# Performance work log

Measured on AMD Instinct MI355X. Metric: run time of the kernel, lower is better.

Reference implementation:

```python
import jax, jax.numpy as jnp
import numpy as np

T = 100000
HDIM = 16
UDIM = 7
HID = 64
DT = 5.0 / 60.0  # 5 minutes in hours


def setup_inputs() -> dict:
    key = jax.random.key(0)
    ks = jax.random.split(key, 12)

    def lin(k, out_d, in_d):
        # torch nn.Linear default init: U(-1/sqrt(in), 1/sqrt(in)); scale-equivalent gaussian is fine for a numeric reference
        bound = 1.0 / np.sqrt(in_d)
        return jax.random.uniform(k, (out_d, in_d), jnp.float32, -bound, bound)

    return {
        "U": jax.random.normal(ks[0], (T, UDIM), jnp.float32),
        "W1": lin(ks[1], HID, HDIM + UDIM),
        "b1": jnp.zeros((HID,), jnp.float32),
        "W2": lin(ks[2], HID, HID),
        "b2": jnp.zeros((HID,), jnp.float32),
        "W3": lin(ks[3], HDIM, HID),
        "b3": jnp.zeros((HDIM,), jnp.float32),
        "wd": lin(ks[4], 1, HDIM).reshape(HDIM),
        "bd": jnp.zeros((), jnp.float32),
        "wt": lin(ks[5], 1, HDIM).reshape(HDIM),
        "bt": jnp.zeros((), jnp.float32),
        "wc": lin(ks[6], 1, HDIM).reshape(HDIM),
        "bc": jnp.zeros((), jnp.float32),
        "h0": jnp.zeros((HDIM,), jnp.float32),
    }


def reference(U, W1, b1, W2, b2, W3, b3, wd, bd, wt, bt, wc, bc, h0):
    dt = jnp.float32(DT)

    def step(h, u):
        # readout at current state (before the Euler step), matching the torch loop order
        d = h @ wd + bd
        tx = h @ wt + bt
        ll = h @ wc + bc
        x = jnp.concatenate([h, u])                    # (HDIM+UDIM,)
        z = jnp.tanh(W1 @ x + b1)                      # (HID,)
        z = jnp.tanh(W2 @ z + b2)                      # (HID,)
        dh = W3 @ z + b3                               # (HDIM,)
        return h + dh * dt, (d, tx, ll)

    hT, (delay, taxi, loglam) = jax.lax.scan(step, h0, U)
    return delay, taxi, loglam, hT.reshape(1, HDIM)
```

## Files before the change

### kernel.cpp

```cpp
#include <hip/hip_runtime.h>

typedef float v2f __attribute__((ext_vector_type(2)));

#define T_STEPS 100000
#define UDIM 7
#define NCHUNK 1562
#define TAIL 32
#define ZSTR 68

__device__ __forceinline__ float tanh_fast(float x) {
    float e = __expf(2.0f * x);
    return 1.0f - 2.0f * __builtin_amdgcn_rcpf(e + 1.0f);
}

__device__ __forceinline__ float readlane_f(float v, int l) {
    return __int_as_float(__builtin_amdgcn_readlane(__float_as_int(v), l));
}

template <int CTRL>
__device__ __forceinline__ float dpp_f(float v) {
    return __int_as_float(__builtin_amdgcn_update_dpp(
        0, __float_as_int(v), CTRL, 0xF, 0xF, true));
}

__global__ __launch_bounds__(64) __attribute__((amdgpu_waves_per_eu(1, 1)))
void node_scan(const float* __restrict__ U,
               const float* __restrict__ W1, const float* __restrict__ b1,
               const float* __restrict__ W2, const float* __restrict__ b2,
               const float* __restrict__ W3, const float* __restrict__ b3,
               const float* __restrict__ wd, const float* __restrict__ bd,
               const float* __restrict__ wt, const float* __restrict__ bt,
               const float* __restrict__ wc, const float* __restrict__ bc,
               const float* __restrict__ h0,
               float* __restrict__ out)
{
    const int lane = threadIdx.x;
    const int g = lane >> 2;
    const int q = lane & 3;
    const float dt = (float)(5.0 / 60.0);

    __shared__ __align__(16) float zbuf[64];
    __shared__ __align__(16) float ubuf[2 * 64 * 8];
    __shared__ __align__(16) float zhist[64 * ZSTR];
    __shared__ __align__(16) float cbuf[3 * 64];
    __shared__ __align__(16) float Msh[64 * 64];

    float w1h[16];
#pragma unroll
    for (int j = 0; j < 16; ++j) w1h[j] = W1[lane * 23 + j];
    v2f W1up[3];
#pragma unroll
    for (int j = 0; j < 3; ++j) {
        W1up[j].x = W1[lane * 23 + 16 + 2 * j];
        W1up[j].y = W1[lane * 23 + 17 + 2 * j];
    }
    const float W1u6 = W1[lane * 23 + 22];
    const float b1r = b1[lane];
    const float b2r = b2[lane];

    v2f W2p[4][8];
#pragma unroll
    for (int d = 0; d < 4; ++d) {
        const int orow = (g << 2) | (q ^ d);
        const float* w2r = W2 + orow * 64 + q * 16;
#pragma unroll
        for (int j = 0; j < 8; ++j) W2p[d][j] = (v2f){ w2r[2 * j], w2r[2 * j + 1] };
    }

    for (int c = 0; c < 64; ++c) {
        float acc = 0.f;
#pragma unroll
        for (int k = 0; k < 16; ++k) acc = fmaf(w1h[k], W3[k * 64 + c], acc);
        Msh[lane * 64 + c] = acc;
    }
    __syncthreads();
    v2f Mp[4][8];
#pragma unroll
    for (int d = 0; d < 4; ++d) {
        const int orow = (g << 2) | (q ^ d);
        const float* mr = Msh + orow * 64 + q * 16;
#pragma unroll
        for (int j = 0; j < 8; ++j) Mp[d][j] = (v2f){ mr[2 * j], mr[2 * j + 1] };
    }
    float m3od = 0.f;
#pragma unroll
    for (int k = 0; k < 16; ++k) m3od = fmaf(w1h[k], b3[k], m3od);

    {
        float cd = 0.f, ct = 0.f, cc = 0.f;
        for (int k = 0; k < 16; ++k) {
            const float w3v = W3[k * 64 + lane];
            cd = fmaf(wd[k], w3v, cd);
            ct = fmaf(wt[k], w3v, ct);
            cc = fmaf(wc[k], w3v, cc);
        }
        cbuf[lane] = cd; cbuf[64 + lane] = ct; cbuf[128 + lane] = cc;
    }
    float rbD = 0.f, rbT = 0.f, rbC = 0.f;
    float rchD = bd[0], rchT = bt[0], rchC = bc[0];
    for (int k = 0; k < 16; ++k) {
        rbD = fmaf(wd[k], b3[k], rbD);  rchD = fmaf(wd[k], h0[k], rchD);
        rbT = fmaf(wt[k], b3[k], rbT);  rchT = fmaf(wt[k], h0[k], rchT);
        rbC = fmaf(wc[k], b3[k], rbC);  rchC = fmaf(wc[k], h0[k], rchC);
    }
    rbD *= dt; rbT *= dt; rbC *= dt;

    float A = 0.f;
    for (int k = 0; k < 16; ++k) A = fmaf(w1h[k], h0[k], A);
    float zacc = 0.f;

#pragma unroll
    for (int r = 0; r < UDIM; ++r) {
        int flat = r * 64 + lane;
        int s = flat / 7, c = flat % 7;
        ubuf[s * 8 + c] = U[flat];
    }
    ubuf[lane * 8 + 7] = 0.f;
    ubuf[512 + lane * 8 + 7] = 0.f;
    __syncthreads();

    float tmp[UDIM];
#pragma unroll
    for (int r = 0; r < UDIM; ++r) tmp[r] = U[448 + r * 64 + lane];

    float uacc;
    {
        float4 ua = *(const float4*)&ubuf[0];
        float4 ub = *(const float4*)&ubuf[4];
        v2f v0 = __builtin_elementwise_fma(W1up[0], (v2f){ua.x, ua.y}, (v2f){0.f, 0.f});
        v0 = __builtin_elementwise_fma(W1up[1], (v2f){ua.z, ua.w}, v0);
        v0 = __builtin_elementwise_fma(W1up[2], (v2f){ub.x, ub.y}, v0);
        uacc = v0.x + v0.y + fmaf(W1u6, ub.z, b1r);
    }

    auto step = [&](int li, int uoff) {
        const float z1 = tanh_fast(A + uacc);
        zbuf[lane] = z1;
        float4 s0 = *(const float4*)&zbuf[q * 16 + 0];
        float4 s1 = *(const float4*)&zbuf[q * 16 + 4];
        float4 s2 = *(const float4*)&zbuf[q * 16 + 8];
        float4 s3 = *(const float4*)&zbuf[q * 16 + 12];

        float4 una = *(const float4*)&ubuf[uoff];
        float4 unb = *(const float4*)&ubuf[uoff + 4];

        v2f e0 = {s0.x, s0.y}, e1 = {s0.z, s0.w};
        v2f e2 = {s1.x, s1.y}, e3 = {s1.z, s1.w};
        v2f e4 = {s2.x, s2.y}, e5 = {s2.z, s2.w};
        v2f e6 = {s3.x, s3.y}, e7 = {s3.z, s3.w};
        v2f c0 = {b2r, 0.f}, c1 = {0.f, 0.f}, c2 = {0.f, 0.f}, c3 = {0.f, 0.f};
        c0 = __builtin_elementwise_fma(W2p[0][0], e0, c0);
        c1 = __builtin_elementwise_fma(W2p[1][0], e0, c1);
        c2 = __builtin_elementwise_fma(W2p[2][0], e0, c2);
        c3 = __builtin_elementwise_fma(W2p[3][0], e0, c3);
        c0 = __builtin_elementwise_fma(W2p[0][1], e1, c0);
        c1 = __builtin_elementwise_fma(W2p[1][1], e1, c1);
        c2 = __builtin_elementwise_fma(W2p[2][1], e1, c2);
        c3 = __builtin_elementwise_fma(W2p[3][1], e1, c3);
        c0 = __builtin_elementwise_fma(W2p[0][2], e2, c0);
        c1 = __builtin_elementwise_fma(W2p[1][2], e2, c1);
        c2 = __builtin_elementwise_fma(W2p[2][2], e2, c2);
        c3 = __builtin_elementwise_fma(W2p[3][2], e2, c3);
        c0 = __builtin_elementwise_fma(W2p[0][3], e3, c0);
        c1 = __builtin_elementwise_fma(W2p[1][3], e3, c1);
        c2 = __builtin_elementwise_fma(W2p[2][3], e3, c2);
        c3 = __builtin_elementwise_fma(W2p[3][3], e3, c3);
        c0 = __builtin_elementwise_fma(W2p[0][4], e4, c0);
        c1 = __builtin_elementwise_fma(W2p[1][4], e4, c1);
        c2 = __builtin_elementwise_fma(W2p[2][4], e4, c2);
        c3 = __builtin_elementwise_fma(W2p[3][4], e4, c3);
        c0 = __builtin_elementwise_fma(W2p[0][5], e5, c0);
        c1 = __builtin_elementwise_fma(W2p[1][5], e5, c1);
        c2 = __builtin_elementwise_fma(W2p[2][5], e5, c2);
        c3 = __builtin_elementwise_fma(W2p[3][5], e5, c3);
        c0 = __builtin_elementwise_fma(W2p[0][6], e6, c0);
        c1 = __builtin_elementwise_fma(W2p[1][6], e6, c1);
        c2 = __builtin_elementwise_fma(W2p[2][6], e6, c2);
        c3 = __builtin_elementwise_fma(W2p[3][6], e6, c3);
        c0 = __builtin_elementwise_fma(W2p[0][7], e7, c0);
        c1 = __builtin_elementwise_fma(W2p[1][7], e7, c1);
        c2 = __builtin_elementwise_fma(W2p[2][7], e7, c2);
        c3 = __builtin_elementwise_fma(W2p[3][7], e7, c3);
        const float P0 = c0.x + c0.y;
        const float P1 = c1.x + c1.y;
        const float P2 = c2.x + c2.y;
        const float P3 = c3.x + c3.y;
        const float Q = P0 + dpp_f<0xB1>(P1) + dpp_f<0x4E>(P2) + dpp_f<0x1B>(P3);
        const float z2 = tanh_fast(Q);
        zhist[li * ZSTR + lane] = z2;
        const float* zrow = &zhist[li * ZSTR + q * 16];
        float4 t0 = *(const float4*)&zrow[0];
        float4 t1 = *(const float4*)&zrow[4];
        float4 t2 = *(const float4*)&zrow[8];
        float4 t3 = *(const float4*)&zrow[12];
        zacc += z2;

        v2f f0 = {t0.x, t0.y}, f1 = {t0.z, t0.w};
        v2f f2 = {t1.x, t1.y}, f3 = {t1.z, t1.w};
        v2f f4 = {t2.x, t2.y}, f5 = {t2.z, t2.w};
        v2f f6 = {t3.x, t3.y}, f7 = {t3.z, t3.w};
        v2f m0 = {m3od, 0.f}, m1 = {0.f, 0.f}, m2 = {0.f, 0.f}, m3 = {0.f, 0.f};
        m0 = __builtin_elementwise_fma(Mp[0][0], f0, m0);
        m1 = __builtin_elementwise_fma(Mp[1][0], f0, m1);
        m2 = __builtin_elementwise_fma(Mp[2][0], f0, m2);
        m3 = __builtin_elementwise_fma(Mp[3][0], f0, m3);
        m0 = __builtin_elementwise_fma(Mp[0][1], f1, m0);
        m1 = __builtin_elementwise_fma(Mp[1][1], f1, m1);
        m2 = __builtin_elementwise_fma(Mp[2][1], f1, m2);
        m3 = __builtin_elementwise_fma(Mp[3][1], f1, m3);
        m0 = __builtin_elementwise_fma(Mp[0][2], f2, m0);
        m1 = __builtin_elementwise_fma(Mp[1][2], f2, m1);
        m2 = __builtin_elementwise_fma(Mp[2][2], f2, m2);
        m3 = __builtin_elementwise_fma(Mp[3][2], f2, m3);
        m0 = __builtin_elementwise_fma(Mp[0][3], f3, m0);
        m1 = __builtin_elementwise_fma(Mp[1][3], f3, m1);
        m2 = __builtin_elementwise_fma(Mp[2][3], f3, m2);
        m3 = __builtin_elementwise_fma(Mp[3][3], f3, m3);
        m0 = __builtin_elementwise_fma(Mp[0][4], f4, m0);
        m1 = __builtin_elementwise_fma(Mp[1][4], f4, m1);
        m2 = __builtin_elementwise_fma(Mp[2][4], f4, m2);
        m3 = __builtin_elementwise_fma(Mp[3][4], f4, m3);
        m0 = __builtin_elementwise_fma(Mp[0][5], f5, m0);
        m1 = __builtin_elementwise_fma(Mp[1][5], f5, m1);
        m2 = __builtin_elementwise_fma(Mp[2][5], f5, m2);
        m3 = __builtin_elementwise_fma(Mp[3][5], f5, m3);
        m0 = __builtin_elementwise_fma(Mp[0][6], f6, m0);
        m1 = __builtin_elementwise_fma(Mp[1][6], f6, m1);
        m2 = __builtin_elementwise_fma(Mp[2][6], f6, m2);
        m3 = __builtin_elementwise_fma(Mp[3][6], f6, m3);
        m0 = __builtin_elementwise_fma(Mp[0][7], f7, m0);
        m1 = __builtin_elementwise_fma(Mp[1][7], f7, m1);
        m2 = __builtin_elementwise_fma(Mp[2][7], f7, m2);
        m3 = __builtin_elementwise_fma(Mp[3][7], f7, m3);
        const float R0 = m0.x + m0.y;
        const float R1 = m1.x + m1.y;
        const float R2 = m2.x + m2.y;
        const float R3 = m3.x + m3.y;
        const float R = R0 + dpp_f<0xB1>(R1) + dpp_f<0x4E>(R2) + dpp_f<0x1B>(R3);
        A = fmaf(dt, R, A);

        v2f uv = __builtin_elementwise_fma(W1up[0], (v2f){una.x, una.y}, (v2f){0.f, 0.f});
        uv = __builtin_elementwise_fma(W1up[1], (v2f){una.z, una.w}, uv);
        uv = __builtin_elementwise_fma(W1up[2], (v2f){unb.x, unb.y}, uv);
        uacc = uv.x + uv.y + fmaf(W1u6, unb.z, b1r);
    };

    auto batch = [&](int t0) {
        const float* zr = &zhist[lane * ZSTR];
        v2f sd = {0.f, 0.f}, st = {0.f, 0.f}, sc = {0.f, 0.f};
#pragma unroll
        for (int qq = 0; qq < 32; ++qq) {
            v2f zv = *(const v2f*)&zr[2 * qq];
            sd = __builtin_elementwise_fma(*(const v2f*)&cbuf[2 * qq],       zv, sd);
            st = __builtin_elementwise_fma(*(const v2f*)&cbuf[64 + 2 * qq],  zv, st);
            sc = __builtin_elementwise_fma(*(const v2f*)&cbuf[128 + 2 * qq], zv, sc);
        }
        float Sd = sd.x + sd.y, St = st.x + st.y, Sc = sc.x + sc.y;
        const float oD = Sd, oT = St, oC = Sc;
#pragma unroll
        for (int dl = 1; dl < 64; dl <<= 1) {
            float ud = __shfl_up(Sd, dl, 64);
            float ut = __shfl_up(St, dl, 64);
            float uc = __shfl_up(Sc, dl, 64);
            if (lane >= dl) { Sd += ud; St += ut; Sc += uc; }
        }
        const int t = t0 + lane;
        if (t < T_STEPS) {
            const float fl = (float)lane;
            out[t]               = fmaf(dt, Sd - oD, rchD) + fl * rbD;
            out[T_STEPS + t]     = fmaf(dt, St - oT, rchT) + fl * rbT;
            out[2 * T_STEPS + t] = fmaf(dt, Sc - oC, rchC) + fl * rbC;
        }
        rchD = fmaf(dt, readlane_f(Sd, 63), rchD) + 64.f * rbD;
        rchT = fmaf(dt, readlane_f(St, 63), rchT) + 64.f * rbT;
        rchC = fmaf(dt, readlane_f(Sc, 63), rchC) + 64.f * rbC;
    };

    for (int cb = 0; cb < NCHUNK; ++cb) {
        const int buf512  = 512 * (cb & 1);
        const int other   = 512 * ((cb + 1) & 1);
#pragma unroll
        for (int r = 0; r < UDIM; ++r) {
            int flat = r * 64 + lane;
            int s = flat / 7, c = flat % 7;
            ubuf[other + s * 8 + c] = tmp[r];
        }
        const int base = (cb + 2) * 448;
#pragma unroll
        for (int r = 0; r < UDIM; ++r) {
            int idx = base + r * 64 + lane;
            if (idx > T_STEPS * UDIM - 1) idx = T_STEPS * UDIM - 1;
            tmp[r] = U[idx];
        }
#pragma unroll 8
        for (int li = 0; li < 64; ++li) {
            const int uoff = (li < 63) ? buf512 + (li + 1) * 8 : other;
            step(li, uoff);
        }
        batch(cb * 64);
    }
    for (int li = 0; li < TAIL; ++li) step(li, (li + 1) * 8);
    batch(NCHUNK * 64);

    zbuf[lane] = zacc;
    float4 za[16];
#pragma unroll
    for (int qq = 0; qq < 16; ++qq) za[qq] = *(const float4*)&zbuf[qq * 4];
    const int row = lane & 15;
    const float* w3r = W3 + row * 64;
    float h0a = 0.f, h1a = 0.f;
#pragma unroll
    for (int qq = 0; qq < 16; ++qq) {
        h0a = fmaf(w3r[4 * qq + 0], za[qq].x, h0a);
        h1a = fmaf(w3r[4 * qq + 1], za[qq].y, h1a);
        h0a = fmaf(w3r[4 * qq + 2], za[qq].z, h0a);
        h1a = fmaf(w3r[4 * qq + 3], za[qq].w, h1a);
    }
    const float hT = h0[row] + dt * (h0a + h1a) + (float)T_STEPS * dt * b3[row];
    if (lane < 16) out[3 * T_STEPS + lane] = hT;
}

extern "C" void kernel_launch(void* const* d_in, const int* in_sizes, int n_in,
                              void* d_out, int out_size, void* d_ws, size_t ws_size,
                              hipStream_t stream) {
    const float* U  = (const float*)d_in[0];
    const float* W1 = (const float*)d_in[1];
    const float* b1 = (const float*)d_in[2];
    const float* W2 = (const float*)d_in[3];
    const float* b2 = (const float*)d_in[4];
    const float* W3 = (const float*)d_in[5];
    const float* b3 = (const float*)d_in[6];
    const float* wd = (const float*)d_in[7];
    const float* bd = (const float*)d_in[8];
    const float* wt = (const float*)d_in[9];
    const float* bt = (const float*)d_in[10];
    const float* wc = (const float*)d_in[11];
    const float* bc = (const float*)d_in[12];
    const float* h0 = (const float*)d_in[13];
    (void)in_sizes; (void)n_in; (void)out_size; (void)d_ws; (void)ws_size;

    node_scan<<<dim3(1), dim3(64), 0, stream>>>(U, W1, b1, W2, b2, W3, b3,
                                                wd, bd, wt, bt, wc, bc, h0,
                                                (float*)d_out);
}
```

Before: 28.55 ms.

## Split recurrence and readout/prefetch into producer-consumer warps with LDS flags

Launches two wavefronts: wave 0 runs only the serial recurrent steps, while wave 1 prefetches U into a triple-buffered LDS ring and computes the readout prefix-scan and output stores for the previous chunk from a double-buffered z history. Workgroup-scope atomic flags with s_sleep spin loops replace the in-line prefetch and batch work. This takes readout and global-memory latency off the critical serial path. The cost is spin-wait overhead, extra LDS, and a risk that the flag handshake stalls the recurrence wave.

```diff
diff --git a/kernel.cpp b/kernel.cpp
--- a/kernel.cpp
+++ b/kernel.cpp
@@ -7,6 +7,7 @@
 #define NCHUNK 1562
 #define TAIL 32
 #define ZSTR 68
+#define ZH (64 * ZSTR)
 
 __device__ __forceinline__ float tanh_fast(float x) {
     float e = __expf(2.0f * x);
@@ -23,7 +24,7 @@
         0, __float_as_int(v), CTRL, 0xF, 0xF, true));
 }
 
-__global__ __launch_bounds__(64) __attribute__((amdgpu_waves_per_eu(1, 1)))
+__global__ __launch_bounds__(128) __attribute__((amdgpu_waves_per_eu(1, 1)))
 void node_scan(const float* __restrict__ U,
                const float* __restrict__ W1, const float* __restrict__ b1,
                const float* __restrict__ W2, const float* __restrict__ b2,
@@ -34,59 +35,51 @@
                const float* __restrict__ h0,
                float* __restrict__ out)
 {
-    const int lane = threadIdx.x;
+    const int tid  = threadIdx.x;
+    const int wv   = tid >> 6;
+    const int lane = tid & 63;
     const int g = lane >> 2;
     const int q = lane & 3;
     const float dt = (float)(5.0 / 60.0);
 
     __shared__ __align__(16) float zbuf[64];
-    __shared__ __align__(16) float ubuf[2 * 64 * 8];
-    __shared__ __align__(16) float zhist[64 * ZSTR];
+    __shared__ __align__(16) float ubuf[3 * 512];
+    __shared__ __align__(16) float zhist[2 * ZH];
     __shared__ __align__(16) float cbuf[3 * 64];
     __shared__ __align__(16) float Msh[64 * 64];
-
-    float w1h[16];
-#pragma unroll
-    for (int j = 0; j < 16; ++j) w1h[j] = W1[lane * 23 + j];
-    v2f W1up[3];
-#pragma unroll
-    for (int j = 0; j < 3; ++j) {
-        W1up[j].x = W1[lane * 23 + 16 + 2 * j];
-        W1up[j].y = W1[lane * 23 + 17 + 2 * j];
-    }
-    const float W1u6 = W1[lane * 23 + 22];
-    const float b1r = b1[lane];
-    const float b2r = b2[lane];
-
+    __shared__ int flg[4];
+
+    if (tid == 0) { flg[0] = 0; flg[1] = 3; flg[2] = 0; }
+
+    float w1h[16]; v2f W1up[3]; float W1u6 = 0.f, b1r = 0.f, b2r = 0.f;
     v2f W2p[4][8];
-#pragma unroll
-    for (int d = 0; d < 4; ++d) {
-        const int orow = (g << 2) | (q ^ d);
-        const float* w2r = W2 + orow * 64 + q * 16;
-#pragma unroll
-        for (int j = 0; j < 8; ++j) W2p[d][j] = (v2f){ w2r[2 * j], w2r[2 * j + 1] };
-    }
-
-    for (int c = 0; c < 64; ++c) {
-        float acc = 0.f;
-#pragma unroll
-        for (int k = 0; k < 16; ++k) acc = fmaf(w1h[k], W3[k * 64 + c], acc);
-        Msh[lane * 64 + c] = acc;
-    }
-    __syncthreads();
-    v2f Mp[4][8];
-#pragma unroll
-    for (int d = 0; d < 4; ++d) {
-        const int orow = (g << 2) | (q ^ d);
-        const float* mr = Msh + orow * 64 + q * 16;
-#pragma unroll
-        for (int j = 0; j < 8; ++j) Mp[d][j] = (v2f){ mr[2 * j], mr[2 * j + 1] };
-    }
-    float m3od = 0.f;
-#pragma unroll
-    for (int k = 0; k < 16; ++k) m3od = fmaf(w1h[k], b3[k], m3od);
-
-    {
+    float rbD = 0.f, rbT = 0.f, rbC = 0.f, rchD = 0.f, rchT = 0.f, rchC = 0.f;
+
+    if (wv == 0) {
+#pragma unroll
+        for (int j = 0; j < 16; ++j) w1h[j] = W1[lane * 23 + j];
+#pragma unroll
+        for (int j = 0; j < 3; ++j) {
+            W1up[j].x = W1[lane * 23 + 16 + 2 * j];
+            W1up[j].y = W1[lane * 23 + 17 + 2 * j];
+        }
+        W1u6 = W1[lane * 23 + 22];
+        b1r = b1[lane];
+        b2r = b2[lane];
+#pragma unroll
+        for (int d = 0; d < 4; ++d) {
+            const int orow = (g << 2) | (q ^ d);
+            const float* w2r = W2 + orow * 64 + q * 16;
+#pragma unroll
+            for (int j = 0; j < 8; ++j) W2p[d][j] = (v2f){ w2r[2 * j], w2r[2 * j + 1] };
+        }
+        for (int c = 0; c < 64; ++c) {
+            float acc = 0.f;
+#pragma unroll
+            for (int k = 0; k < 16; ++k) acc = fmaf(w1h[k], W3[k * 64 + c], acc);
+            Msh[lane * 64 + c] = acc;
+        }
+    } else {
         float cd = 0.f, ct = 0.f, cc = 0.f;
         for (int k = 0; k < 16; ++k) {
             const float w3v = W3[k * 64 + lane];
@@ -95,229 +88,256 @@
             cc = fmaf(wc[k], w3v, cc);
         }
         cbuf[lane] = cd; cbuf[64 + lane] = ct; cbuf[128 + lane] = cc;
+        rchD = bd[0]; rchT = bt[0]; rchC = bc[0];
+        for (int k = 0; k < 16; ++k) {
+            rbD = fmaf(wd[k], b3[k], rbD);  rchD = fmaf(wd[k], h0[k], rchD);
+            rbT = fmaf(wt[k], b3[k], rbT);  rchT = fmaf(wt[k], h0[k], rchT);
+            rbC = fmaf(wc[k], b3[k], rbC);  rchC = fmaf(wc[k], h0[k], rchC);
+        }
+        rbD *= dt; rbT *= dt; rbC *= dt;
+#pragma unroll
+        for (int c = 0; c < 3; ++c) {
+            const int base = c * 448, dst = c * 512;
+#pragma unroll
+            for (int r = 0; r < UDIM; ++r) {
+                int flat = r * 64 + lane;
+                int s = flat / 7, cc2 = flat % 7;
+                ubuf[dst + s * 8 + cc2] = U[base + flat];
+            }
+            ubuf[dst + lane * 8 + 7] = 0.f;
+        }
     }
-    float rbD = 0.f, rbT = 0.f, rbC = 0.f;
-    float rchD = bd[0], rchT = bt[0], rchC = bc[0];
-    for (int k = 0; k < 16; ++k) {
-        rbD = fmaf(wd[k], b3[k], rbD);  rchD = fmaf(wd[k], h0[k], rchD);
-        rbT = fmaf(wt[k], b3[k], rbT);  rchT = fmaf(wt[k], h0[k], rchT);
-        rbC = fmaf(wc[k], b3[k], rbC);  rchC = fmaf(wc[k], h0[k], rchC);
+    __syncthreads();
+
+    if (wv == 0) {
+        v2f Mp[4][8];
+#pragma unroll
+        for (int d = 0; d < 4; ++d) {
+            const int orow = (g << 2) | (q ^ d);
+            const float* mr = Msh + orow * 64 + q * 16;
+#pragma unroll
+            for (int j = 0; j < 8; ++j) Mp[d][j] = (v2f){ mr[2 * j], mr[2 * j + 1] };
+        }
+        float m3od = 0.f;
+#pragma unroll
+        for (int k = 0; k < 16; ++k) m3od = fmaf(w1h[k], b3[k], m3od);
+        float A = 0.f;
+        for (int k = 0; k < 16; ++k) A = fmaf(w1h[k], h0[k], A);
+        float zacc = 0.f;
+        float uacc;
+        {
+            float4 ua = *(const float4*)&ubuf[0];
+            float4 ub = *(const float4*)&ubuf[4];
+            v2f v0 = __builtin_elementwise_fma(W1up[0], (v2f){ua.x, ua.y}, (v2f){0.f, 0.f});
+            v0 = __builtin_elementwise_fma(W1up[1], (v2f){ua.z, ua.w}, v0);
+            v0 = __builtin_elementwise_fma(W1up[2], (v2f){ub.x, ub.y}, v0);
+            uacc = v0.x + v0.y + fmaf(W1u6, ub.z, b1r);
+        }
+
+        auto step = [&](int li, int uoff, int zbase) {
+            const float z1 = tanh_fast(A + uacc);
+            zbuf[lane] = z1;
+            float4 s0 = *(const float4*)&zbuf[q * 16 + 0];
+            float4 s1 = *(const float4*)&zbuf[q * 16 + 4];
+            float4 s2 = *(const float4*)&zbuf[q * 16 + 8];
+            float4 s3 = *(const float4*)&zbuf[q * 16 + 12];
+
+            float4 una = *(const float4*)&ubuf[uoff];
+            float4 unb = *(const float4*)&ubuf[uoff + 4];
+
+            v2f e0 = {s0.x, s0.y}, e1 = {s0.z, s0.w};
+            v2f e2 = {s1.x, s1.y}, e3 = {s1.z, s1.w};
+            v2f e4 = {s2.x, s2.y}, e5 = {s2.z, s2.w};
+            v2f e6 = {s3.x, s3.y}, e7 = {s3.z, s3.w};
+            v2f c0 = {b2r, 0.f}, c1 = {0.f, 0.f}, c2 = {0.f, 0.f}, c3 = {0.f, 0.f};
+            c0 = __builtin_elementwise_fma(W2p[0][0], e0, c0);
+            c1 = __builtin_elementwise_fma(W2p[1][0], e0, c1);
+            c2 = __builtin_elementwise_fma(W2p[2][0], e0, c2);
+            c3 = __builtin_elementwise_fma(W2p[3][0], e0, c3);
+            c0 = __builtin_elementwise_fma(W2p[0][1], e1, c0);
+            c1 = __builtin_elementwise_fma(W2p[1][1], e1, c1);
+            c2 = __builtin_elementwise_fma(W2p[2][1], e1, c2);
+            c3 = __builtin_elementwise_fma(W2p[3][1], e1, c3);
+            c0 = __builtin_elementwise_fma(W2p[0][2], e2, c0);
+            c1 = __builtin_elementwise_fma(W2p[1][2], e2, c1);
+            c2 = __builtin_elementwise_fma(W2p[2][2], e2, c2);
+            c3 = __builtin_elementwise_fma(W2p[3][2], e2, c3);
+            c0 = __builtin_elementwise_fma(W2p[0][3], e3, c0);
+            c1 = __builtin_elementwise_fma(W2p[1][3], e3, c1);
+            c2 = __builtin_elementwise_fma(W2p[2][3], e3, c2);
+            c3 = __builtin_elementwise_fma(W2p[3][3], e3, c3);
+            c0 = __builtin_elementwise_fma(W2p[0][4], e4, c0);
+            c1 = __builtin_elementwise_fma(W2p[1][4], e4, c1);
+            c2 = __builtin_elementwise_fma(W2p[2][4], e4, c2);
+            c3 = __builtin_elementwise_fma(W2p[3][4], e4, c3);
+            c0 = __builtin_elementwise_fma(W2p[0][5], e5, c0);
+            c1 = __builtin_elementwise_fma(W2p[1][5], e5, c1);
+            c2 = __builtin_elementwise_fma(W2p[2][5], e5, c2);
+            c3 = __builtin_elementwise_fma(W2p[3][5], e5, c3);
+            c0 = __builtin_elementwise_fma(W2p[0][6], e6, c0);
+            c1 = __builtin_elementwise_fma(W2p[1][6], e6, c1);
+            c2 = __builtin_elementwise_fma(W2p[2][6], e6, c2);
+            c3 = __builtin_elementwise_fma(W2p[3][6], e6, c3);
+            c0 = __builtin_elementwise_fma(W2p[0][7], e7, c0);
+            c1 = __builtin_elementwise_fma(W2p[1][7], e7, c1);
+            c2 = __builtin_elementwise_fma(W2p[2][7], e7, c2);
+            c3 = __builtin_elementwise_fma(W2p[3][7], e7, c3);
+            const float P0 = c0.x + c0.y;
+            const float P1 = c1.x + c1.y;
+            const float P2 = c2.x + c2.y;
+            const float P3 = c3.x + c3.y;
+            const float Q = P0 + dpp_f<0xB1>(P1) + dpp_f<0x4E>(P2) + dpp_f<0x1B>(P3);
+            const float z2 = tanh_fast(Q);
+            zhist[zbase + li * ZSTR + lane] = z2;
+            const float* zrow = &zhist[zbase + li * ZSTR + q * 16];
+            float4 t0 = *(const float4*)&zrow[0];
+            float4 t1 = *(const float4*)&zrow[4];
+            float4 t2 = *(const float4*)&zrow[8];
+            float4 t3 = *(const float4*)&zrow[12];
+            zacc += z2;
+
+            v2f f0 = {t0.x, t0.y}, f1 = {t0.z, t0.w};
+            v2f f2 = {t1.x, t1.y}, f3 = {t1.z, t1.w};
+            v2f f4 = {t2.x, t2.y}, f5 = {t2.z, t2.w};
+            v2f f6 = {t3.x, t3.y}, f7 = {t3.z, t3.w};
+            v2f m0 = {m3od, 0.f}, m1 = {0.f, 0.f}, m2 = {0.f, 0.f}, m3 = {0.f, 0.f};
+            m0 = __builtin_elementwise_fma(Mp[0][0], f0, m0);
+            m1 = __builtin_elementwise_fma(Mp[1][0], f0, m1);
+            m2 = __builtin_elementwise_fma(Mp[2][0], f0, m2);
+            m3 = __builtin_elementwise_fma(Mp[3][0], f0, m3);
+            m0 = __builtin_elementwise_fma(Mp[0][1], f1, m0);
+            m1 = __builtin_elementwise_fma(Mp[1][1], f1, m1);
+            m2 = __builtin_elementwise_fma(Mp[2][1], f1, m2);
+            m3 = __builtin_elementwise_fma(Mp[3][1], f1, m3);
+            m0 = __builtin_elementwise_fma(Mp[0][2], f2, m0);
+            m1 = __builtin_elementwise_fma(Mp[1][2], f2, m1);
+            m2 = __builtin_elementwise_fma(Mp[2][2], f2, m2);
+            m3 = __builtin_elementwise_fma(Mp[3][2], f2, m3);
+            m0 = __builtin_elementwise_fma(Mp[0][3], f3, m0);
+            m1 = __builtin_elementwise_fma(Mp[1][3], f3, m1);
+            m2 = __builtin_elementwise_fma(Mp[2][3], f3, m2);
+            m3 = __builtin_elementwise_fma(Mp[3][3], f3, m3);
+            m0 = __builtin_elementwise_fma(Mp[0][4], f4, m0);
+            m1 = __builtin_elementwise_fma(Mp[1][4], f4, m1);
+            m2 = __builtin_elementwise_fma(Mp[2][4], f4, m2);
+            m3 = __builtin_elementwise_fma(Mp[3][4], f4, m3);
+            m0 = __builtin_elementwise_fma(Mp[0][5], f5, m0);
+            m1 = __builtin_elementwise_fma(Mp[1][5], f5, m1);
+            m2 = __builtin_elementwise_fma(Mp[2][5], f5, m2);
+            m3 = __builtin_elementwise_fma(Mp[3][5], f5, m3);
+            m0 = __builtin_elementwise_fma(Mp[0][6], f6, m0);
+            m1 = __builtin_elementwise_fma(Mp[1][6], f6, m1);
+            m2 = __builtin_elementwise_fma(Mp[2][6], f6, m2);
+            m3 = __builtin_elementwise_fma(Mp[3][6], f6, m3);
+            m0 = __builtin_elementwise_fma(Mp[0][7], f7, m0);
+            m1 = __builtin_elementwise_fma(Mp[1][7], f7, m1);
+            m2 = __builtin_elementwise_fma(Mp[2][7], f7, m2);
+            m3 = __builtin_elementwise_fma(Mp[3][7], f7, m3);
+            const float R0 = m0.x + m0.y;
+            const float R1 = m1.x + m1.y;
+            const float R2 = m2.x + m2.y;
+            const float R3 = m3.x + m3.y;
+            const float R = R0 + dpp_f<0xB1>(R1) + dpp_f<0x4E>(R2) + dpp_f<0x1B>(R3);
+            A = fmaf(dt, R, A);
+
+            v2f uv = __builtin_elementwise_fma(W1up[0], (v2f){una.x, una.y}, (v2f){0.f, 0.f});
+            uv = __builtin_elementwise_fma(W1up[1], (v2f){una.z, una.w}, uv);
+            uv = __builtin_elementwise_fma(W1up[2], (v2f){unb.x, unb.y}, uv);
+            uacc = uv.x + uv.y + fmaf(W1u6, unb.z, b1r);
+        };
+
+        for (int cb = 0; cb <= NCHUNK; ++cb) {
+            const int need_staged = (cb + 2 < NCHUNK + 1) ? cb + 2 : NCHUNK + 1;
+            while (__hip_atomic_load(&flg[1], __ATOMIC_ACQUIRE,
+                                     __HIP_MEMORY_SCOPE_WORKGROUP) < need_staged)
+                __builtin_amdgcn_s_sleep(1);
+            while (__hip_atomic_load(&flg[2], __ATOMIC_ACQUIRE,
+                                     __HIP_MEMORY_SCOPE_WORKGROUP) < cb - 1)
+                __builtin_amdgcn_s_sleep(1);
+            const int zbase = (cb & 1) * ZH;
+            const int ub = (cb % 3) * 512;
+            if (cb < NCHUNK) {
+                const int un = ((cb + 1) % 3) * 512;
+#pragma unroll 8
+                for (int li = 0; li < 64; ++li) {
+                    const int uoff = (li < 63) ? ub + (li + 1) * 8 : un;
+                    step(li, uoff, zbase);
+                }
+            } else {
+                for (int li = 0; li < TAIL; ++li) step(li, ub + (li + 1) * 8, zbase);
+            }
+            __hip_atomic_store(&flg[0], cb + 1, __ATOMIC_RELEASE,
+                               __HIP_MEMORY_SCOPE_WORKGROUP);
+        }
+
+        zbuf[lane] = zacc;
+        float4 za[16];
+#pragma unroll
+        for (int qq = 0; qq < 16; ++qq) za[qq] = *(const float4*)&zbuf[qq * 4];
+        const int row = lane & 15;
+        const float* w3r = W3 + row * 64;
+        float h0a = 0.f, h1a = 0.f;
+#pragma unroll
+        for (int qq = 0; qq < 16; ++qq) {
+            h0a = fmaf(w3r[4 * qq + 0], za[qq].x, h0a);
+            h1a = fmaf(w3r[4 * qq + 1], za[qq].y, h1a);
+            h0a = fmaf(w3r[4 * qq + 2], za[qq].z, h0a);
+            h1a = fmaf(w3r[4 * qq + 3], za[qq].w, h1a);
+        }
+        const float hT = h0[row] + dt * (h0a + h1a) + (float)T_STEPS * dt * b3[row];
+        if (lane < 16) out[3 * T_STEPS + lane] = hT;
+    } else {
+        for (int cb = 0; cb <= NCHUNK; ++cb) {
+            while (__hip_atomic_load(&flg[0], __ATOMIC_ACQUIRE,
+                                     __HIP_MEMORY_SCOPE_WORKGROUP) < cb + 1)
+                __builtin_amdgcn_s_sleep(8);
+            if (cb + 3 <= NCHUNK) {
+                const int dst = ((cb + 3) % 3) * 512;
+                const int base = (cb + 3) * 448;
+#pragma unroll
+                for (int r = 0; r < UDIM; ++r) {
+                    int idx = base + r * 64 + lane;
+                    if (idx > T_STEPS * UDIM - 1) idx = T_STEPS * UDIM - 1;
+                    const float val = U[idx];
+                    int flat = r * 64 + lane;
+                    int s = flat / 7, c = flat % 7;
+                    ubuf[dst + s * 8 + c] = val;
+                }
+                __hip_atomic_store(&flg[1], cb + 4, __ATOMIC_RELEASE,
+                                   __HIP_MEMORY_SCOPE_WORKGROUP);
+            }
+            const float* zr = &zhist[(cb & 1) * ZH + lane * ZSTR];
+            v2f sd = {0.f, 0.f}, st = {0.f, 0.f}, sc = {0.f, 0.f};
+#pragma unroll
+            for (int qq = 0; qq < 32; ++qq) {
+                v2f zv = *(const v2f*)&zr[2 * qq];
+                sd = __builtin_elementwise_fma(*(const v2f*)&cbuf[2 * qq],       zv, sd);
+                st = __builtin_elementwise_fma(*(const v2f*)&cbuf[64 + 2 * qq],  zv, st);
+                sc = __builtin_elementwise_fma(*(const v2f*)&cbuf[128 + 2 * qq], zv, sc);
+            }
+            float Sd = sd.x + sd.y, St = st.x + st.y, Sc = sc.x + sc.y;
+            const float oD = Sd, oT = St, oC = Sc;
+#pragma unroll
+            for (int dl = 1; dl < 64; dl <<= 1) {
+                float ud = __shfl_up(Sd, dl, 64);
+                float ut = __shfl_up(St, dl, 64);
+                float uc = __shfl_up(Sc, dl, 64);
+                if (lane >= dl) { Sd += ud; St += ut; Sc += uc; }
+            }
+            const int t = cb * 64 + lane;
+            if (t < T_STEPS) {
+                const float fl = (float)lane;
+                out[t]               = fmaf(dt, Sd - oD, rchD) + fl * rbD;
+                out[T_STEPS + t]     = fmaf(dt, St - oT, rchT) + fl * rbT;
+                out[2 * T_STEPS + t] = fmaf(dt, Sc - oC, rchC) + fl * rbC;
+            }
+            rchD = fmaf(dt, readlane_f(Sd, 63), rchD) + 64.f * rbD;
+            rchT = fmaf(dt, readlane_f(St, 63), rchT) + 64.f * rbT;
+            rchC = fmaf(dt, readlane_f(Sc, 63), rchC) + 64.f * rbC;
+            __hip_atomic_store(&flg[2], cb + 1, __ATOMIC_RELEASE,
+                               __HIP_MEMORY_SCOPE_WORKGROUP);
+        }
     }
-    rbD *= dt; rbT *= dt; rbC *= dt;
-
-    float A = 0.f;
-    for (int k = 0; k < 16; ++k) A = fmaf(w1h[k], h0[k], A);
-    float zacc = 0.f;
-
-#pragma unroll
-    for (int r = 0; r < UDIM; ++r) {
-        int flat = r * 64 + lane;
-        int s = flat / 7, c = flat % 7;
-        ubuf[s * 8 + c] = U[flat];
-    }
-    ubuf[lane * 8 + 7] = 0.f;
-    ubuf[512 + lane * 8 + 7] = 0.f;
-    __syncthreads();
-
-    float tmp[UDIM];
-#pragma unroll
-    for (int r = 0; r < UDIM; ++r) tmp[r] = U[448 + r * 64 + lane];
-
-    float uacc;
-    {
-        float4 ua = *(const float4*)&ubuf[0];
-        float4 ub = *(const float4*)&ubuf[4];
-        v2f v0 = __builtin_elementwise_fma(W1up[0], (v2f){ua.x, ua.y}, (v2f){0.f, 0.f});
-        v0 = __builtin_elementwise_fma(W1up[1], (v2f){ua.z, ua.w}, v0);
-        v0 = __builtin_elementwise_fma(W1up[2], (v2f){ub.x, ub.y}, v0);
-        uacc = v0.x + v0.y + fmaf(W1u6, ub.z, b1r);
-    }
-
-    auto step = [&](int li, int uoff) {
-        const float z1 = tanh_fast(A + uacc);
-        zbuf[lane] = z1;
-        float4 s0 = *(const float4*)&zbuf[q * 16 + 0];
-        float4 s1 = *(const float4*)&zbuf[q * 16 + 4];
-        float4 s2 = *(const float4*)&zbuf[q * 16 + 8];
-        float4 s3 = *(const float4*)&zbuf[q * 16 + 12];
-
-        float4 una = *(const float4*)&ubuf[uoff];
-        float4 unb = *(const float4*)&ubuf[uoff + 4];
-
-        v2f e0 = {s0.x, s0.y}, e1 = {s0.z, s0.w};
-        v2f e2 = {s1.x, s1.y}, e3 = {s1.z, s1.w};
-        v2f e4 = {s2.x, s2.y}, e5 = {s2.z, s2.w};
-        v2f e6 = {s3.x, s3.y}, e7 = {s3.z, s3.w};
-        v2f c0 = {b2r, 0.f}, c1 = {0.f, 0.f}, c2 = {0.f, 0.f}, c3 = {0.f, 0.f};
-        c0 = __builtin_elementwise_fma(W2p[0][0], e0, c0);
-        c1 = __builtin_elementwise_fma(W2p[1][0], e0, c1);
-        c2 = __builtin_elementwise_fma(W2p[2][0], e0, c2);
-        c3 = __builtin_elementwise_fma(W2p[3][0], e0, c3);
-        c0 = __builtin_elementwise_fma(W2p[0][1], e1, c0);
-        c1 = __builtin_elementwise_fma(W2p[1][1], e1, c1);
-        c2 = __builtin_elementwise_fma(W2p[2][1], e1, c2);
-        c3 = __builtin_elementwise_fma(W2p[3][1], e1, c3);
-        c0 = __builtin_elementwise_fma(W2p[0][2], e2, c0);
-        c1 = __builtin_elementwise_fma(W2p[1][2], e2, c1);
-        c2 = __builtin_elementwise_fma(W2p[2][2], e2, c2);
-        c3 = __builtin_elementwise_fma(W2p[3][2], e2, c3);
-        c0 = __builtin_elementwise_fma(W2p[0][3], e3, c0);
-        c1 = __builtin_elementwise_fma(W2p[1][3], e3, c1);
-        c2 = __builtin_elementwise_fma(W2p[2][3], e3, c2);
-        c3 = __builtin_elementwise_fma(W2p[3][3], e3, c3);
-        c0 = __builtin_elementwise_fma(W2p[0][4], e4, c0);
-        c1 = __builtin_elementwise_fma(W2p[1][4], e4, c1);
-        c2 = __builtin_elementwise_fma(W2p[2][4], e4, c2);
-        c3 = __builtin_elementwise_fma(W2p[3][4], e4, c3);
-        c0 = __builtin_elementwise_fma(W2p[0][5], e5, c0);
-        c1 = __builtin_elementwise_fma(W2p[1][5], e5, c1);
-        c2 = __builtin_elementwise_fma(W2p[2][5], e5, c2);
-        c3 = __builtin_elementwise_fma(W2p[3][5], e5, c3);
-        c0 = __builtin_elementwise_fma(W2p[0][6], e6, c0);
-        c1 = __builtin_elementwise_fma(W2p[1][6], e6, c1);
-        c2 = __builtin_elementwise_fma(W2p[2][6], e6, c2);
-        c3 = __builtin_elementwise_fma(W2p[3][6], e6, c3);
-        c0 = __builtin_elementwise_fma(W2p[0][7], e7, c0);
-        c1 = __builtin_elementwise_fma(W2p[1][7], e7, c1);
-        c2 = __builtin_elementwise_fma(W2p[2][7], e7, c2);
-        c3 = __builtin_elementwise_fma(W2p[3][7], e7, c3);
-        const float P0 = c0.x + c0.y;
-        const float P1 = c1.x + c1.y;
-        const float P2 = c2.x + c2.y;
-        const float P3 = c3.x + c3.y;
-        const float Q = P0 + dpp_f<0xB1>(P1) + dpp_f<0x4E>(P2) + dpp_f<0x1B>(P3);
-        const float z2 = tanh_fast(Q);
-        zhist[li * ZSTR + lane] = z2;
-        const float* zrow = &zhist[li * ZSTR + q * 16];
-        float4 t0 = *(const float4*)&zrow[0];
-        float4 t1 = *(const float4*)&zrow[4];
-        float4 t2 = *(const float4*)&zrow[8];
-        float4 t3 = *(const float4*)&zrow[12];
-        zacc += z2;
-
-        v2f f0 = {t0.x, t0.y}, f1 = {t0.z, t0.w};
-        v2f f2 = {t1.x, t1.y}, f3 = {t1.z, t1.w};
-        v2f f4 = {t2.x, t2.y}, f5 = {t2.z, t2.w};
-        v2f f6 = {t3.x, t3.y}, f7 = {t3.z, t3.w};
-        v2f m0 = {m3od, 0.f}, m1 = {0.f, 0.f}, m2 = {0.f, 0.f}, m3 = {0.f, 0.f};
-        m0 = __builtin_elementwise_fma(Mp[0][0], f0, m0);
-        m1 = __builtin_elementwise_fma(Mp[1][0], f0, m1);
-        m2 = __builtin_elementwise_fma(Mp[2][0], f0, m2);
-        m3 = __builtin_elementwise_fma(Mp[3][0], f0, m3);
-        m0 = __builtin_elementwise_fma(Mp[0][1], f1, m0);
-        m1 = __builtin_elementwise_fma(Mp[1][1], f1, m1);
-        m2 = __builtin_elementwise_fma(Mp[2][1], f1, m2);
-        m3 = __builtin_elementwise_fma(Mp[3][1], f1, m3);
-        m0 = __builtin_elementwise_fma(Mp[0][2], f2, m0);
-        m1 = __builtin_elementwise_fma(Mp[1][2], f2, m1);
-        m2 = __builtin_elementwise_fma(Mp[2][2], f2, m2);
-        m3 = __builtin_elementwise_fma(Mp[3][2], f2, m3);
-        m0 = __builtin_elementwise_fma(Mp[0][3], f3, m0);
-        m1 = __builtin_elementwise_fma(Mp[1][3], f3, m1);
-        m2 = __builtin_elementwise_fma(Mp[2][3], f3, m2);
-        m3 = __builtin_elementwise_fma(Mp[3][3], f3, m3);
-        m0 = __builtin_elementwise_fma(Mp[0][4], f4, m0);
-        m1 = __builtin_elementwise_fma(Mp[1][4], f4, m1);
-        m2 = __builtin_elementwise_fma(Mp[2][4], f4, m2);
-        m3 = __builtin_elementwise_fma(Mp[3][4], f4, m3);
-        m0 = __builtin_elementwise_fma(Mp[0][5], f5, m0);
-        m1 = __builtin_elementwise_fma(Mp[1][5], f5, m1);
-        m2 = __builtin_elementwise_fma(Mp[2][5], f5, m2);
-        m3 = __builtin_elementwise_fma(Mp[3][5], f5, m3);
-        m0 = __builtin_elementwise_fma(Mp[0][6], f6, m0);
-        m1 = __builtin_elementwise_fma(Mp[1][6], f6, m1);
-        m2 = __builtin_elementwise_fma(Mp[2][6], f6, m2);
-        m3 = __builtin_elementwise_fma(Mp[3][6], f6, m3);
-        m0 = __builtin_elementwise_fma(Mp[0][7], f7, m0);
-        m1 = __builtin_elementwise_fma(Mp[1][7], f7, m1);
-        m2 = __builtin_elementwise_fma(Mp[2][7], f7, m2);
-        m3 = __builtin_elementwise_fma(Mp[3][7], f7, m3);
-        const float R0 = m0.x + m0.y;
-        const float R1 = m1.x + m1.y;
-        const float R2 = m2.x + m2.y;
-        const float R3 = m3.x + m3.y;
-        const float R = R0 + dpp_f<0xB1>(R1) + dpp_f<0x4E>(R2) + dpp_f<0x1B>(R3);
-        A = fmaf(dt, R, A);
-
-        v2f uv = __builtin_elementwise_fma(W1up[0], (v2f){una.x, una.y}, (v2f){0.f, 0.f});
-        uv = __builtin_elementwise_fma(W1up[1], (v2f){una.z, una.w}, uv);
-        uv = __builtin_elementwise_fma(W1up[2], (v2f){unb.x, unb.y}, uv);
-        uacc = uv.x + uv.y + fmaf(W1u6, unb.z, b1r);
-    };
-
-    auto batch = [&](int t0) {
-        const float* zr = &zhist[lane * ZSTR];
-        v2f sd = {0.f, 0.f}, st = {0.f, 0.f}, sc = {0.f, 0.f};
-#pragma unroll
-        for (int qq = 0; qq < 32; ++qq) {
-            v2f zv = *(const v2f*)&zr[2 * qq];
-            sd = __builtin_elementwise_fma(*(const v2f*)&cbuf[2 * qq],       zv, sd);
-            st = __builtin_elementwise_fma(*(const v2f*)&cbuf[64 + 2 * qq],  zv, st);
-            sc = __builtin_elementwise_fma(*(const v2f*)&cbuf[128 + 2 * qq], zv, sc);
-        }
-        float Sd = sd.x + sd.y, St = st.x + st.y, Sc = sc.x + sc.y;
-        const float oD = Sd, oT = St, oC = Sc;
-#pragma unroll
-        for (int dl = 1; dl < 64; dl <<= 1) {
-            float ud = __shfl_up(Sd, dl, 64);
-            float ut = __shfl_up(St, dl, 64);
-            float uc = __shfl_up(Sc, dl, 64);
-            if (lane >= dl) { Sd += ud; St += ut; Sc += uc; }
-        }
-        const int t = t0 + lane;
-        if (t < T_STEPS) {
-            const float fl = (float)lane;
-            out[t]               = fmaf(dt, Sd - oD, rchD) + fl * rbD;
-            out[T_STEPS + t]     = fmaf(dt, St - oT, rchT) + fl * rbT;
-            out[2 * T_STEPS + t] = fmaf(dt, Sc - oC, rchC) + fl * rbC;
-        }
-        rchD = fmaf(dt, readlane_f(Sd, 63), rchD) + 64.f * rbD;
-        rchT = fmaf(dt, readlane_f(St, 63), rchT) + 64.f * rbT;
-        rchC = fmaf(dt, readlane_f(Sc, 63), rchC) + 64.f * rbC;
-    };
-
-    for (int cb = 0; cb < NCHUNK; ++cb) {
-        const int buf512  = 512 * (cb & 1);
-        const int other   = 512 * ((cb + 1) & 1);
-#pragma unroll
-        for (int r = 0; r < UDIM; ++r) {
-            int flat = r * 64 + lane;
-            int s = flat / 7, c = flat % 7;
-            ubuf[other + s * 8 + c] = tmp[r];
-        }
-        const int base = (cb + 2) * 448;
-#pragma unroll
-        for (int r = 0; r < UDIM; ++r) {
-            int idx = base + r * 64 + lane;
-            if (idx > T_STEPS * UDIM - 1) idx = T_STEPS * UDIM - 1;
-            tmp[r] = U[idx];
-        }
-#pragma unroll 8
-        for (int li = 0; li < 64; ++li) {
-            const int uoff = (li < 63) ? buf512 + (li + 1) * 8 : other;
-            step(li, uoff);
-        }
-        batch(cb * 64);
-    }
-    for (int li = 0; li < TAIL; ++li) step(li, (li + 1) * 8);
-    batch(NCHUNK * 64);
-
-    zbuf[lane] = zacc;
-    float4 za[16];
-#pragma unroll
-    for (int qq = 0; qq < 16; ++qq) za[qq] = *(const float4*)&zbuf[qq * 4];
-    const int row = lane & 15;
-    const float* w3r = W3 + row * 64;
-    float h0a = 0.f, h1a = 0.f;
-#pragma unroll
-    for (int qq = 0; qq < 16; ++qq) {
-        h0a = fmaf(w3r[4 * qq + 0], za[qq].x, h0a);
-        h1a = fmaf(w3r[4 * qq + 1], za[qq].y, h1a);
-        h0a = fmaf(w3r[4 * qq + 2], za[qq].z, h0a);
-        h1a = fmaf(w3r[4 * qq + 3], za[qq].w, h1a);
-    }
-    const float hT = h0[row] + dt * (h0a + h1a) + (float)T_STEPS * dt * b3[row];
-    if (lane < 16) out[3 * T_STEPS + lane] = hT;
 }
 
 extern "C" void kernel_launch(void* const* d_in, const int* in_sizes, int n_in,
@@ -339,7 +359,7 @@
     const float* h0 = (const float*)d_in[13];
     (void)in_sizes; (void)n_in; (void)out_size; (void)d_ws; (void)ws_size;
 
-    node_scan<<<dim3(1), dim3(64), 0, stream>>>(U, W1, b1, W2, b2, W3, b3,
-                                                wd, bd, wt, bt, wc, bc, h0,
-                                                (float*)d_out);
-}
+    node_scan<<<dim3(1), dim3(128), 0, stream>>>(U, W1, b1, W2, b2, W3, b3,
+                                                 wd, bd, wt, bt, wc, bc, h0,
+                                                 (float*)d_out);
+}
```

Result: faster. 27.81 ms (-2.6%).
